# Kernel tuning notes

Measured on AMD Instinct MI355X. Metric: run time of the kernel, lower is better.

## Reference

```python
import jax, jax.numpy as jnp
import numpy as np

NUM_HEADS = 16
ROPE_BASE = 10000.0


def rotate_half(x):
    d = x.shape[-1] // 2
    return jnp.concatenate([-x[..., d:], x[..., :d]], axis=-1)


def setup_inputs() -> dict:
    key = jax.random.key(0)
    ks = jax.random.split(key, 6)
    B, S, H = 2, 2048, 1024
    scale = 1.0 / np.sqrt(H)  # ~xavier for square matrices
    x = jax.random.normal(ks[0], (B, S, H), dtype=jnp.float32)
    Wq = jax.random.normal(ks[1], (H, H), dtype=jnp.float32) * scale
    Wk = jax.random.normal(ks[2], (H, H), dtype=jnp.float32) * scale
    Wv = jax.random.normal(ks[3], (H, H), dtype=jnp.float32) * scale
    Wo = jax.random.normal(ks[4], (H, H), dtype=jnp.float32) * scale
    # learnable bias, tril-initialized as in the torch module
    bias = jnp.tril(jax.random.normal(ks[5], (S, S), dtype=jnp.float32) * 0.02)
    return {"x": x, "Wq": Wq, "Wk": Wk, "Wv": Wv, "Wo": Wo, "bias": bias}


def reference(x, Wq, Wk, Wv, Wo, bias):
    B, S, H = x.shape
    nh = NUM_HEADS
    hd = H // nh

    # projections (torch Linear: y = x @ W.T), split heads -> [B, nh, S, hd]
    q = (x @ Wq.T).reshape(B, S, nh, hd).transpose(0, 2, 1, 3)
    k = (x @ Wk.T).reshape(B, S, nh, hd).transpose(0, 2, 1, 3)
    v = (x @ Wv.T).reshape(B, S, nh, hd).transpose(0, 2, 1, 3)

    # rotary embeddings, position_ids = arange(S)
    inv_freq = 1.0 / (ROPE_BASE ** (jnp.arange(0, hd, 2, dtype=jnp.float32) / hd))
    t = jnp.arange(S, dtype=jnp.float32)
    freqs = t[:, None] * inv_freq[None, :]          # [S, hd/2]
    emb = jnp.concatenate([freqs, freqs], axis=-1)  # [S, hd]
    cos = jnp.cos(emb).astype(x.dtype)
    sin = jnp.sin(emb).astype(x.dtype)
    q = q * cos + rotate_half(q) * sin
    k = k * cos + rotate_half(k) * sin

    # scores + learnable bias + causal mask
    scores = jnp.einsum('bhqd,bhkd->bhqk', q, k) / np.float32(np.sqrt(hd))
    scores = scores + bias[:S, :S][None, None, :, :]
    causal = jnp.tril(jnp.ones((S, S), dtype=bool))
    scores = jnp.where(causal, scores, -jnp.inf)

    attn = jax.nn.softmax(scores, axis=-1)
    out = jnp.einsum('bhqk,bhkd->bhqd', attn, v)
    out = out.transpose(0, 2, 1, 3).reshape(B, S, H)
    return out @ Wo.T, attn
```

## Files before the change

### kernel.cpp

```cpp
#include <hip/hip_runtime.h>
#include <hip/hip_bf16.h>
#include <math.h>


typedef __attribute__((ext_vector_type(8))) short bx8;
typedef __attribute__((ext_vector_type(4))) short sx4;
typedef __attribute__((ext_vector_type(4))) float fx4;
typedef __attribute__((ext_vector_type(4))) float f4v;

#define MFMA_BF16(a, b, c) __builtin_amdgcn_mfma_f32_16x16x32_bf16(a, b, c, 0, 0, 0)
#define LOG2E 1.44269504088896340736f

__device__ __forceinline__ short f2bf(float f) {
    union { float f; unsigned u; } v; v.f = f;
    unsigned u = v.u;
    u += 0x7fffu + ((u >> 16) & 1u);
    return (short)(u >> 16);
}
__device__ __forceinline__ float u2f(unsigned u) {
    union { unsigned u; float f; } v; v.u = u; return v.f;
}
__device__ __forceinline__ float bf2f(short s) {
    return u2f(((unsigned)(unsigned short)s) << 16);
}

__device__ __forceinline__ bx8 pack8(f4v a, f4v b) {
    bx8 r;
    r[0] = f2bf(a[0]); r[1] = f2bf(a[1]); r[2] = f2bf(a[2]); r[3] = f2bf(a[3]);
    r[4] = f2bf(b[0]); r[5] = f2bf(b[1]); r[6] = f2bf(b[2]); r[7] = f2bf(b[3]);
    return r;
}

__device__ __forceinline__ void gload_lds16(const short* g, short* l) {
    __builtin_amdgcn_global_load_lds(
        (const __attribute__((address_space(1))) void*)g,
        (__attribute__((address_space(3))) void*)l, 16, 0, 0);
}

__global__ __launch_bounds__(256) void cast_kernel(
        const float* __restrict__ x, const float* __restrict__ Wq,
        const float* __restrict__ Wk, const float* __restrict__ Wv,
        const float* __restrict__ Wo, const float* __restrict__ bias,
        short* __restrict__ dst, short* __restrict__ bias_bf)
{
    const size_t M1 = 1u << 20;
    if (blockIdx.x < 4096) {
        const size_t e0 = ((size_t)blockIdx.x * 256 + threadIdx.x) * 8;
        const float* src; size_t off;
        if (e0 < 4 * M1) { src = x; off = e0; }
        else {
            const int j = (int)((e0 - 4 * M1) >> 20);
            src = (j == 0) ? Wq : (j == 1) ? Wk : (j == 2) ? Wv : Wo;
            off = (e0 - 4 * M1) & (M1 - 1);
        }
        f4v a = *(const f4v*)(src + off);
        f4v b = *(const f4v*)(src + off + 4);
        *(bx8*)(dst + e0) = pack8(a, b);
    } else {
        const size_t e0 = ((size_t)(blockIdx.x - 4096) * 256 + threadIdx.x) * 8;
        f4v a = *(const f4v*)(bias + e0);
        f4v b = *(const f4v*)(bias + e0 + 4);
        #pragma unroll
        for (int i = 0; i < 4; ++i) { a[i] *= LOG2E; b[i] *= LOG2E; }
        *(bx8*)(bias_bf + e0) = pack8(a, b);
    }
}

__global__ void rope_table_kernel(float* __restrict__ cosT, float* __restrict__ sinT) {
    int i = blockIdx.x * 256 + threadIdx.x;
    if (i >= 2048 * 64) return;
    int s = i >> 6, d = i & 63;
    int fi = d & 31;
    float inv_freq = powf(10000.0f, -(float)fi / 32.0f);
    float ang = (float)s * inv_freq;
    cosT[i] = cosf(ang);
    sinT[i] = sinf(ang);
}

template<int OUTPROJ>
__global__ __launch_bounds__(256) void gemm128(
        const short* __restrict__ A, const short* __restrict__ W0,
        const short* __restrict__ W1, const short* __restrict__ W2,
        const float* __restrict__ cosT, const float* __restrict__ sinT,
        void* __restrict__ Out)
{
    __shared__ __align__(16) char SMEM[128 * 130 * 2];
    short (*As)[64]  = (short(*)[64])SMEM;
    short (*Bs)[64]  = (short(*)[64])(SMEM + 16384);
    short (*Cs)[130] = (short(*)[130])SMEM;

    const int bm = blockIdx.x, bn = blockIdx.y, z = blockIdx.z;
    const short* W = OUTPROJ ? W0 : (z == 0 ? W0 : (z == 1 ? W1 : W2));
    const int tid = threadIdx.x, w = tid >> 6, lane = tid & 63;
    const int cl = lane & 15, lg = lane >> 4;
    const int srow = lane >> 3;
    const int schunk = (lane & 7) ^ srow;

    fx4 acc[4][4];
    #pragma unroll
    for (int mi = 0; mi < 4; ++mi)
        #pragma unroll
        for (int ni = 0; ni < 4; ++ni) acc[mi][ni] = (fx4){0.f, 0.f, 0.f, 0.f};

    const int wr = (w >> 1) * 64, wc = (w & 1) * 64;

    for (int k0 = 0; k0 < 1024; k0 += 64) {
        __syncthreads();
        #pragma unroll
        for (int i = 0; i < 4; ++i) {
            const int rbase = w * 32 + i * 8;
            gload_lds16(A + (size_t)(bm * 128 + rbase + srow) * 1024 + k0 + schunk * 8,
                        &As[rbase][0]);
            gload_lds16(W + (size_t)(bn * 128 + rbase + srow) * 1024 + k0 + schunk * 8,
                        &Bs[rbase][0]);
        }
        __syncthreads();
        #pragma unroll
        for (int kk = 0; kk < 2; ++kk) {
            bx8 af[4], bf[4];
            #pragma unroll
            for (int i = 0; i < 4; ++i) {
                const int ra = wr + i * 16 + cl;
                af[i] = *(const bx8*)&As[ra][((kk * 4 + lg) ^ (ra & 7)) * 8];
                const int rb = wc + i * 16 + cl;
                bf[i] = *(const bx8*)&Bs[rb][((kk * 4 + lg) ^ (rb & 7)) * 8];
            }
            #pragma unroll
            for (int mi = 0; mi < 4; ++mi)
                #pragma unroll
                for (int ni = 0; ni < 4; ++ni)
                    acc[mi][ni] = MFMA_BF16(af[mi], bf[ni], acc[mi][ni]);
        }
    }

    if constexpr (OUTPROJ) {
        #pragma unroll
        for (int mi = 0; mi < 4; ++mi) {
            #pragma unroll
            for (int reg = 0; reg < 4; ++reg) {
                const int r = bm * 128 + wr + mi * 16 + (lg << 2) + reg;
                #pragma unroll
                for (int ni = 0; ni < 4; ++ni) {
                    const int col = bn * 128 + wc + ni * 16 + cl;
                    ((float*)Out)[(size_t)r * 1024 + col] = acc[mi][ni][reg];
                }
            }
        }
    } else {
        __syncthreads();
        #pragma unroll
        for (int mi = 0; mi < 4; ++mi) {
            #pragma unroll
            for (int reg = 0; reg < 4; ++reg) {
                const int rl = wr + mi * 16 + (lg << 2) + reg;
                const int s = (bm * 128 + rl) & 2047;
                #pragma unroll
                for (int ni = 0; ni < 4; ++ni) {
                    const int cloc = wc + ni * 16 + cl;
                    const int d = cloc & 63;
                    float v = acc[mi][ni][reg];
                    if (z <= 1) {
                        const float cs = cosT[s * 64 + d], sn = sinT[s * 64 + d];
                        const float partner = acc[mi][ni ^ 2][reg];
                        const float rot = (d < 32) ? -partner : partner;
                        v = v * cs + rot * sn;
                        if (z == 0) v *= 0.125f * LOG2E;
                    }
                    Cs[rl][cloc] = f2bf(v);
                }
            }
        }
        __syncthreads();
        #pragma unroll
        for (int i = 0; i < 8; ++i) {
            const int u = tid + i * 256;
            const int chunk = u & 7, hh = (u >> 3) & 1, sl = u >> 4;
            bx8 vv = *(const bx8*)&Cs[sl][hh * 64 + chunk * 8];
            const int r = bm * 128 + sl;
            const int bb = r >> 11, ss = r & 2047;
            short* dst = (short*)Out + (size_t)z * 32 * 2048 * 64
                       + (size_t)((bb * 16 + bn * 2 + hh) * 2048 + ss) * 64 + chunk * 8;
            *(bx8*)dst = vv;
        }
    }
}

__global__ __launch_bounds__(512, 4) void attn_kernel(
        const short* __restrict__ Q, const short* __restrict__ K,
        const short* __restrict__ V, const short* __restrict__ bias_bf,
        float* __restrict__ attn_out, short* __restrict__ o_buf)
{
    const int S = 2048;
    const int bid = blockIdx.x;
    const int bh = (bid & 7) * 4 + ((bid >> 3) & 3);
    const int qt = (bid < 256) ? (15 - (bid >> 5)) : ((bid >> 5) - 8);
    const int h = bh & 15, b = bh >> 4;
    const int tid = threadIdx.x, w = tid >> 6, lane = tid & 63;
    const int cl = lane & 15, lg = lane >> 4;
    const size_t base = (size_t)bh * S * 64;
    const int NT = 2 * qt + 2;

    __shared__ short Ks[2][64][64];
    __shared__ short Vt[2][64][72];
    __shared__ short P[8][16][136];

    const int krow8 = lane >> 3, kchk = (lane & 7) ^ krow8;
    const int vrow = tid >> 3, vd0 = (tid & 7) * 8;

    const short* qp = Q + base + (size_t)(qt * 128 + w * 16 + cl) * 64 + lg * 8;
    const bx8 qf0 = *(const bx8*)qp;
    const bx8 qf1 = *(const bx8*)(qp + 32);
    const int qr  = qt * 128 + w * 16 + cl;
    const int qrmin = qt * 128 + w * 16;
    const int sq0 = qt * 128 + w * 16 + (lg << 2);
    const short* brow = bias_bf + (size_t)qr * 2048;
    const size_t strip_base = ((size_t)bh * S + qt * 128 + w * 16) * S;

#define STAGEK(BUF, t)                                                            \
    gload_lds16(K + base + (size_t)((t) * 64 + w * 8 + krow8) * 64 + kchk * 8,    \
                &Ks[BUF][w * 8][0]);

#define LOADB(BR, t)                                                              \
    { _Pragma("unroll") for (int n = 0; n < 4; ++n)                               \
        BR[n] = *(const sx4*)(brow + (t) * 64 + n * 16 + (lg << 2)); }

#define QKT(BUF, SACC)                                                            \
    { const int cs_ = cl & 7;                                                     \
      const fx4 zf = (fx4){0.f, 0.f, 0.f, 0.f};                                   \
      __builtin_amdgcn_s_setprio(1);                                              \
      _Pragma("unroll") for (int n = 0; n < 4; ++n) {                             \
        bx8 a0 = *(const bx8*)&Ks[BUF][n * 16 + cl][(lg ^ cs_) * 8];              \
        bx8 a1 = *(const bx8*)&Ks[BUF][n * 16 + cl][((4 + lg) ^ cs_) * 8];        \
        SACC[n] = MFMA_BF16(a0, qf0, zf);                                         \
        SACC[n] = MFMA_BF16(a1, qf1, SACC[n]); }                                  \
      __builtin_amdgcn_s_setprio(0); }

#define COMP_A(BUF, BR, t)                                                        \
    { fx4 sacc[4]; QKT(BUF, sacc);                                                \
      if ((t) * 64 + 63 <= qrmin) {                    \
        _Pragma("unroll") for (int n = 0; n < 4; ++n)                             \
          _Pragma("unroll") for (int e = 0; e < 4; ++e)                           \
            lsum[n] += exp2f(sacc[n][e] + bf2f(BR[n][e]));                        \
      } else {                                                                    \
        _Pragma("unroll") for (int n = 0; n < 4; ++n)                             \
          _Pragma("unroll") for (int e = 0; e < 4; ++e) {                         \
            const int kc = (t) * 64 + n * 16 + (lg << 2) + e;                     \
            const float sv = sacc[n][e] + bf2f(BR[n][e]);                         \
            lsum[n] += (kc <= qr) ? exp2f(sv) : 0.f; }                            \
      } }

#define LOADVr(V0, t)                                                             \
    V0 = *(const bx8*)(V + base + (size_t)((t) * 64 + vrow) * 64 + vd0);

#define VSTORE(V0, BUF)                                                           \
    { _Pragma("unroll") for (int j = 0; j < 8; ++j) Vt[BUF][vd0 + j][vrow] = V0[j]; }

#define COMP_B(KBUF, BR, VBUF, t)                                                 \
    { fx4 sacc[4]; QKT(KBUF, sacc);                                               \
      if ((t) * 64 + 63 <= qrmin) {                    \
        _Pragma("unroll") for (int n = 0; n < 4; ++n) {                           \
          sx4 pb;                                                                 \
          _Pragma("unroll") for (int e = 0; e < 4; ++e)                           \
            pb[e] = f2bf(exp2f(sacc[n][e] + bf2f(BR[n][e]) - L2));                \
          *(sx4*)&P[w][cl][((t) & 1) * 64 + n * 16 + (lg << 2)] = pb; }           \
      } else {                                                                    \
        _Pragma("unroll") for (int n = 0; n < 4; ++n) {                           \
          sx4 pb;                                                                 \
          _Pragma("unroll") for (int e = 0; e < 4; ++e) {                         \
            const int kc = (t) * 64 + n * 16 + (lg << 2) + e;                     \
            const float sv = sacc[n][e] + bf2f(BR[n][e]);                         \
            const float p = (kc <= qr) ? exp2f(sv - L2) : 0.f;                    \
            pb[e] = f2bf(p); }                                                    \
          *(sx4*)&P[w][cl][((t) & 1) * 64 + n * 16 + (lg << 2)] = pb; }           \
      }                                                                           \
      __builtin_amdgcn_s_setprio(1);                                              \
      _Pragma("unroll") for (int kk = 0; kk < 2; ++kk) {                          \
        bx8 pa = *(const bx8*)&P[w][cl][((t) & 1) * 64 + kk * 32 + lg * 8];       \
        _Pragma("unroll") for (int n = 0; n < 4; ++n) {                           \
          bx8 vb = *(const bx8*)&Vt[VBUF][n * 16 + cl][kk * 32 + lg * 8];         \
          oacc[n] = MFMA_BF16(pa, vb, oacc[n]); } }                               \
      __builtin_amdgcn_s_setprio(0); }

#define FLUSH2(tp)                                                                \
    { _Pragma("unroll") for (int rp = 0; rp < 16; rp += 2) {                      \
        const int row = rp + (lane >> 5), col = (lane & 31) * 4;                  \
        const unsigned* ps = (const unsigned*)&P[w][row][col];                    \
        const unsigned px = ps[0], py = ps[1];                                    \
        f4v o; o[0] = u2f(px << 16); o[1] = u2f(px & 0xffff0000u);                \
        o[2] = u2f(py << 16); o[3] = u2f(py & 0xffff0000u);                       \
        __builtin_nontemporal_store(o,                                            \
            (f4v*)(attn_out + strip_base + (size_t)row * S + (tp) * 64 + col)); } }

    float lsum[4] = {0.f, 0.f, 0.f, 0.f};

    {
        sx4 bA[4], bB[4];
        STAGEK(0, 0); LOADB(bA, 0);
        __syncthreads();
        for (int t = 0; t + 1 < NT; t += 2) {
            STAGEK(1, t + 1); LOADB(bB, t + 1);
            COMP_A(0, bA, t);
            __syncthreads();
            if (t + 2 < NT) { STAGEK(0, t + 2); LOADB(bA, t + 2); }
            COMP_A(1, bB, t + 1);
            __syncthreads();
        }
    }

    float l = (lsum[0] + lsum[1]) + (lsum[2] + lsum[3]);
    l += __shfl_xor(l, 16);
    l += __shfl_xor(l, 32);
    const float L2 = __log2f(l);

    fx4 oacc[4];
    #pragma unroll
    for (int n = 0; n < 4; n++) oacc[n] = (fx4){0.f, 0.f, 0.f, 0.f};

    sx4 bA[4], bB[4];
    bx8 vA0, vB0;
    STAGEK(0, 0); LOADB(bA, 0); LOADVr(vA0, 0);
    __syncthreads();
    VSTORE(vA0, 0);
    __syncthreads();
    for (int t = 0; t + 1 < NT; t += 2) {
        STAGEK(1, t + 1); LOADB(bB, t + 1); LOADVr(vB0, t + 1);
        COMP_B(0, bA, 0, t);
        VSTORE(vB0, 1);
        __syncthreads();
        if (t + 2 < NT) { STAGEK(0, t + 2); LOADB(bA, t + 2); LOADVr(vA0, t + 2); }
        COMP_B(1, bB, 1, t + 1);
        FLUSH2(t);
        if (t + 2 < NT) VSTORE(vA0, 0);
        __syncthreads();
    }

    #pragma unroll
    for (int reg = 0; reg < 4; reg++) {
        const int sq = sq0 + reg;
        #pragma unroll
        for (int n = 0; n < 4; n++) {
            const int d = n * 16 + cl;
            o_buf[(size_t)(b * 2048 + sq) * 1024 + h * 64 + d] = f2bf(oacc[n][reg]);
        }
    }

    const int c0 = (qt + 1) * 128;
    if (c0 < S) {
        const f4v z = (f4v){0.f, 0.f, 0.f, 0.f};
        for (int r = w; r < 128; r += 8) {
            float* dst = attn_out + ((size_t)bh * S + qt * 128 + r) * S;
            for (int cc = c0 + lane * 4; cc < S; cc += 256)
                __builtin_nontemporal_store(z, (f4v*)(dst + cc));
        }
    }
#undef STAGEK
#undef LOADB
#undef QKT
#undef COMP_A
#undef LOADVr
#undef VSTORE
#undef COMP_B
#undef FLUSH2
}

extern "C" void kernel_launch(void* const* d_in, const int* in_sizes, int n_in,
                              void* d_out, int out_size, void* d_ws, size_t ws_size,
                              hipStream_t stream) {
    const float* x    = (const float*)d_in[0];
    const float* Wq   = (const float*)d_in[1];
    const float* Wk   = (const float*)d_in[2];
    const float* Wv   = (const float*)d_in[3];
    const float* Wo   = (const float*)d_in[4];
    const float* bias = (const float*)d_in[5];

    float* out  = (float*)d_out;
    float* attn = out + (size_t)2 * 2048 * 1024;

    char* ws = (char*)d_ws;
    const size_t M1 = 1u << 20;
    short* x_bf    = (short*)ws;
    short* wq_bf   = x_bf + 4 * M1;
    short* wk_bf   = wq_bf + M1;
    short* wv_bf   = wk_bf + M1;
    short* wo_bf   = wv_bf + M1;
    short* bias_bf = wo_bf + M1;
    float* cosT    = (float*)(ws + 24 * M1);
    float* sinT    = cosT + 2048 * 64;
    short* q_rope  = (short*)(ws + 25 * M1);
    short* k_rope  = q_rope + 4 * M1;
    short* v_bf    = k_rope + 4 * M1;
    short* o_buf   = x_bf;

    cast_kernel<<<6144, 256, 0, stream>>>(x, Wq, Wk, Wv, Wo, bias, x_bf, bias_bf);
    rope_table_kernel<<<512, 256, 0, stream>>>(cosT, sinT);
    gemm128<0><<<dim3(32, 8, 3), 256, 0, stream>>>(x_bf, wq_bf, wk_bf, wv_bf,
                                                   cosT, sinT, q_rope);
    attn_kernel<<<512, 512, 0, stream>>>(q_rope, k_rope, v_bf, bias_bf, attn, o_buf);
    gemm128<1><<<dim3(32, 8, 1), 256, 0, stream>>>(o_buf, wo_bf, wo_bf, wo_bf,
                                                   cosT, sinT, out);
}
```

Measured before the change: 248.9 us.

## Write V transposed from projection GEMM and stage it via async LDS loads

The QKV projection epilogue now writes V in a transposed [bh][d][s] layout, so the attention kernel can stage V tiles into shared memory with the same direct global-to-LDS load and XOR swizzle used for K. This removes the per-iteration register load and scalar transposing store of V into LDS, along with one barrier in the prologue. The cost is a strided, column-gathering read from the shared tile in the GEMM epilogue for the V slice.

```diff
diff --git a/kernel.cpp b/kernel.cpp
--- a/kernel.cpp
+++ b/kernel.cpp
@@ -171,23 +171,39 @@
             }
         }
         __syncthreads();
-        #pragma unroll
-        for (int i = 0; i < 8; ++i) {
-            const int u = tid + i * 256;
-            const int chunk = u & 7, hh = (u >> 3) & 1, sl = u >> 4;
-            bx8 vv = *(const bx8*)&Cs[sl][hh * 64 + chunk * 8];
-            const int r = bm * 128 + sl;
-            const int bb = r >> 11, ss = r & 2047;
-            short* dst = (short*)Out + (size_t)z * 32 * 2048 * 64
-                       + (size_t)((bb * 16 + bn * 2 + hh) * 2048 + ss) * 64 + chunk * 8;
-            *(bx8*)dst = vv;
+        if (z == 2) {
+            #pragma unroll
+            for (int i = 0; i < 8; ++i) {
+                const int u = tid + i * 256;
+                const int c = u & 15, d = (u >> 4) & 63, hh = u >> 10;
+                bx8 vv;
+                #pragma unroll
+                for (int j = 0; j < 8; ++j) vv[j] = Cs[c * 8 + j][hh * 64 + d];
+                const int r0 = bm * 128 + c * 8;
+                const int bb = r0 >> 11, ss = r0 & 2047;
+                short* dst = (short*)Out + (size_t)2 * 32 * 2048 * 64
+                           + ((size_t)(bb * 16 + bn * 2 + hh) * 64 + d) * 2048 + ss;
+                *(bx8*)dst = vv;
+            }
+        } else {
+            #pragma unroll
+            for (int i = 0; i < 8; ++i) {
+                const int u = tid + i * 256;
+                const int chunk = u & 7, hh = (u >> 3) & 1, sl = u >> 4;
+                bx8 vv = *(const bx8*)&Cs[sl][hh * 64 + chunk * 8];
+                const int r = bm * 128 + sl;
+                const int bb = r >> 11, ss = r & 2047;
+                short* dst = (short*)Out + (size_t)z * 32 * 2048 * 64
+                           + (size_t)((bb * 16 + bn * 2 + hh) * 2048 + ss) * 64 + chunk * 8;
+                *(bx8*)dst = vv;
+            }
         }
     }
 }
 
 __global__ __launch_bounds__(512, 4) void attn_kernel(
         const short* __restrict__ Q, const short* __restrict__ K,
-        const short* __restrict__ V, const short* __restrict__ bias_bf,
+        const short* __restrict__ Vt_g, const short* __restrict__ bias_bf,
         float* __restrict__ attn_out, short* __restrict__ o_buf)
 {
     const int S = 2048;
@@ -198,14 +214,14 @@
     const int tid = threadIdx.x, w = tid >> 6, lane = tid & 63;
     const int cl = lane & 15, lg = lane >> 4;
     const size_t base = (size_t)bh * S * 64;
+    const size_t vbase = (size_t)bh * 64 * S;
     const int NT = 2 * qt + 2;
 
     __shared__ short Ks[2][64][64];
-    __shared__ short Vt[2][64][72];
+    __shared__ short Vt[2][64][64];
     __shared__ short P[8][16][136];
 
     const int krow8 = lane >> 3, kchk = (lane & 7) ^ krow8;
-    const int vrow = tid >> 3, vd0 = (tid & 7) * 8;
 
     const short* qp = Q + base + (size_t)(qt * 128 + w * 16 + cl) * 64 + lg * 8;
     const bx8 qf0 = *(const bx8*)qp;
@@ -219,6 +235,10 @@
 #define STAGEK(BUF, t)                                                            \
     gload_lds16(K + base + (size_t)((t) * 64 + w * 8 + krow8) * 64 + kchk * 8,    \
                 &Ks[BUF][w * 8][0]);
+
+#define STAGEV(BUF, t)                                                            \
+    gload_lds16(Vt_g + vbase + (size_t)(w * 8 + krow8) * 2048 + (t) * 64 + kchk * 8, \
+                &Vt[BUF][w * 8][0]);
 
 #define LOADB(BR, t)                                                              \
     { _Pragma("unroll") for (int n = 0; n < 4; ++n)                               \
@@ -248,12 +268,6 @@
             const float sv = sacc[n][e] + bf2f(BR[n][e]);                         \
             lsum[n] += (kc <= qr) ? exp2f(sv) : 0.f; }                            \
       } }
-
-#define LOADVr(V0, t)                                                             \
-    V0 = *(const bx8*)(V + base + (size_t)((t) * 64 + vrow) * 64 + vd0);
-
-#define VSTORE(V0, BUF)                                                           \
-    { _Pragma("unroll") for (int j = 0; j < 8; ++j) Vt[BUF][vd0 + j][vrow] = V0[j]; }
 
 #define COMP_B(KBUF, BR, VBUF, t)                                                 \
     { fx4 sacc[4]; QKT(KBUF, sacc);                                               \
@@ -274,11 +288,13 @@
           *(sx4*)&P[w][cl][((t) & 1) * 64 + n * 16 + (lg << 2)] = pb; }           \
       }                                                                           \
       __builtin_amdgcn_s_setprio(1);                                              \
-      _Pragma("unroll") for (int kk = 0; kk < 2; ++kk) {                          \
-        bx8 pa = *(const bx8*)&P[w][cl][((t) & 1) * 64 + kk * 32 + lg * 8];       \
-        _Pragma("unroll") for (int n = 0; n < 4; ++n) {                           \
-          bx8 vb = *(const bx8*)&Vt[VBUF][n * 16 + cl][kk * 32 + lg * 8];         \
-          oacc[n] = MFMA_BF16(pa, vb, oacc[n]); } }                               \
+      { const int cs_ = cl & 7;                                                   \
+        _Pragma("unroll") for (int kk = 0; kk < 2; ++kk) {                        \
+          bx8 pa = *(const bx8*)&P[w][cl][((t) & 1) * 64 + kk * 32 + lg * 8];     \
+          _Pragma("unroll") for (int n = 0; n < 4; ++n) {                         \
+            const int R = n * 16 + cl;                                            \
+            bx8 vb = *(const bx8*)&Vt[VBUF][R][(((kk * 4 + lg)) ^ (R & 7)) * 8];  \
+            oacc[n] = MFMA_BF16(pa, vb, oacc[n]); } } }                           \
       __builtin_amdgcn_s_setprio(0); }
 
 #define FLUSH2(tp)                                                                \
@@ -317,20 +333,15 @@
     for (int n = 0; n < 4; n++) oacc[n] = (fx4){0.f, 0.f, 0.f, 0.f};
 
     sx4 bA[4], bB[4];
-    bx8 vA0, vB0;
-    STAGEK(0, 0); LOADB(bA, 0); LOADVr(vA0, 0);
-    __syncthreads();
-    VSTORE(vA0, 0);
+    STAGEK(0, 0); STAGEV(0, 0); LOADB(bA, 0);
     __syncthreads();
     for (int t = 0; t + 1 < NT; t += 2) {
-        STAGEK(1, t + 1); LOADB(bB, t + 1); LOADVr(vB0, t + 1);
+        STAGEK(1, t + 1); STAGEV(1, t + 1); LOADB(bB, t + 1);
         COMP_B(0, bA, 0, t);
-        VSTORE(vB0, 1);
-        __syncthreads();
-        if (t + 2 < NT) { STAGEK(0, t + 2); LOADB(bA, t + 2); LOADVr(vA0, t + 2); }
+        __syncthreads();
+        if (t + 2 < NT) { STAGEK(0, t + 2); STAGEV(0, t + 2); LOADB(bA, t + 2); }
         COMP_B(1, bB, 1, t + 1);
         FLUSH2(t);
-        if (t + 2 < NT) VSTORE(vA0, 0);
         __syncthreads();
     }
 
@@ -354,11 +365,10 @@
         }
     }
 #undef STAGEK
+#undef STAGEV
 #undef LOADB
 #undef QKT
 #undef COMP_A
-#undef LOADVr
-#undef VSTORE
 #undef COMP_B
 #undef FLUSH2
 }
@@ -388,14 +398,14 @@
     float* sinT    = cosT + 2048 * 64;
     short* q_rope  = (short*)(ws + 25 * M1);
     short* k_rope  = q_rope + 4 * M1;
-    short* v_bf    = k_rope + 4 * M1;
+    short* vT_bf   = k_rope + 4 * M1;
     short* o_buf   = x_bf;
 
     cast_kernel<<<6144, 256, 0, stream>>>(x, Wq, Wk, Wv, Wo, bias, x_bf, bias_bf);
     rope_table_kernel<<<512, 256, 0, stream>>>(cosT, sinT);
     gemm128<0><<<dim3(32, 8, 3), 256, 0, stream>>>(x_bf, wq_bf, wk_bf, wv_bf,
                                                    cosT, sinT, q_rope);
-    attn_kernel<<<512, 512, 0, stream>>>(q_rope, k_rope, v_bf, bias_bf, attn, o_buf);
+    attn_kernel<<<512, 512, 0, stream>>>(q_rope, k_rope, vT_bf, bias_bf, attn, o_buf);
     gemm128<1><<<dim3(32, 8, 1), 256, 0, stream>>>(o_buf, wo_bf, wo_bf, wo_bf,
                                                    cosT, sinT, out);
 }
```

Result: no change. 244.6 us (-1.7%).
